# Kernel tuning notes

Hardware: AMD Instinct MI355X
Metric: run time of the kernel (lower is better)

## Reference

```python
import jax, jax.numpy as jnp
import numpy as np

S, B, E, H = 2048, 2, 1024, 16
D = E // H


def setup_inputs() -> dict:
    key = jax.random.key(0)
    k1, k2, k3, k4 = jax.random.split(key, 4)
    x = jax.random.normal(k1, (S, B, E), dtype=jnp.float32)
    # xavier_uniform for [3E, E] and [O, E]
    lim_qkv = float(np.sqrt(6.0 / (3 * E + E)))
    lim_out = float(np.sqrt(6.0 / (E + E)))
    w_qkv = jax.random.uniform(k2, (3 * E, E), jnp.float32, -lim_qkv, lim_qkv)
    b_qkv = jnp.zeros((3 * E,), jnp.float32)
    w_out = jax.random.uniform(k3, (E, E), jnp.float32, -lim_out, lim_out)
    b_out = jnp.zeros((E,), jnp.float32)
    return {"x": x, "w_qkv": w_qkv, "b_qkv": b_qkv, "w_out": w_out, "b_out": b_out}


def reference(x, w_qkv, b_qkv, w_out, b_out):
    # x: [S, B, E] (seq-first, as in the torch module)
    s, b, e = x.shape
    scaling = jnp.asarray(np.sqrt(D), x.dtype)
    qkv = jnp.einsum('sbe,fe->sbf', x, w_qkv) + b_qkv          # [S,B,3E]
    q, k, v = jnp.split(qkv, 3, axis=-1)
    q = q.reshape(s, b, H, D)
    k = k.reshape(s, b, H, D)
    v = v.reshape(s, b, H, D)
    # scores [B,H,S,S]; note original divides by sqrt(head_dim)
    scores = jnp.einsum('sbhd,tbhd->bhst', q, k) / scaling
    attn_w = jax.nn.softmax(scores.astype(jnp.float32), axis=-1).astype(scores.dtype)
    # dropout p=0.1 is identity in eval mode (training=False)
    attn = jnp.einsum('bhst,tbhd->sbhd', attn_w, v).reshape(s, b, e)
    out = jnp.einsum('sbe,oe->sbo', attn, w_out) + b_out        # [S,B,O]
    attn_avg = attn_w.mean(axis=1)                              # [B,S,S]
    return out, attn_avg
```

## Files before the change

kernel.cpp:

```cpp
#include <hip/hip_runtime.h>

#define SEQ   2048
#define BATCH 2
#define NH    16
#define HD    64
#define EMB   1024

#define QSCALE 0.18033688011112042f

using bf16x8 = __attribute__((ext_vector_type(8))) short;
using f32x4  = __attribute__((ext_vector_type(4))) float;
using f32x16 = __attribute__((ext_vector_type(16))) float;

__device__ __forceinline__ unsigned short f2bf(float f) {
  unsigned int u = __float_as_uint(f);
  u += 0x7FFFu + ((u >> 16) & 1u);
  return (unsigned short)(u >> 16);
}
__device__ __forceinline__ unsigned pk_bf16(float lo, float hi) {
  unsigned r;
  asm("v_cvt_pk_bf16_f32 %0, %1, %2" : "=v"(r) : "v"(lo), "v"(hi));
  return r;
}
__device__ __forceinline__ void gload16(const void* g, void* l) {
  __builtin_amdgcn_global_load_lds(
      (const __attribute__((address_space(1))) unsigned int*)g,
      (__attribute__((address_space(3))) unsigned int*)l, 16, 0, 0);
}

__global__ __launch_bounds__(256) void cvt_f32_bf16(const float* __restrict__ in,
                                                    unsigned short* __restrict__ out,
                                                    int n4) {
  int i = blockIdx.x * 256 + threadIdx.x;
  if (i < n4) {
    float4 v = reinterpret_cast<const float4*>(in)[i];
    ushort4 o;
    o.x = f2bf(v.x); o.y = f2bf(v.y); o.z = f2bf(v.z); o.w = f2bf(v.w);
    reinterpret_cast<ushort4*>(out)[i] = o;
  }
}

template <int EPI>
__global__ __launch_bounds__(256) void gemm_bt(
    const unsigned short* __restrict__ A,
    const unsigned short* __restrict__ B,
    const float* __restrict__ bias,
    float* __restrict__ Cf,
    unsigned short* __restrict__ Qb,
    unsigned short* __restrict__ Kb,
    unsigned short* __restrict__ VTb,
    int M, int N, int K) {
  __shared__ int4 As[128][8];
  __shared__ int4 Bs[128][8];
  const int tid = threadIdx.x;
  const int wid = tid >> 6, lane = tid & 63;
  const int wm = wid >> 1, wn = wid & 1;
  const int lg = lane >> 4, lr = lane & 15;
  const int lr8 = lane >> 3;
  const int lc8 = (lane & 7) ^ lr8;
  const int row0 = blockIdx.x * 128, col0 = blockIdx.y * 128;
  f32x4 acc[4][4] = {};
  for (int k0 = 0; k0 < K; k0 += 64) {
#pragma unroll
    for (int i = 0; i < 4; i++) {
      const int rb = wid * 32 + i * 8;
      gload16(&A[(size_t)(row0 + rb + lr8) * K + k0 + lc8 * 8], &As[rb][0]);
      gload16(&B[(size_t)(col0 + rb + lr8) * K + k0 + lc8 * 8], &Bs[rb][0]);
    }
    __syncthreads();
#pragma unroll
    for (int ks = 0; ks < 2; ks++) {
      bf16x8 af[4], bfr[4];
#pragma unroll
      for (int mi = 0; mi < 4; mi++) {
        int r = wm * 64 + mi * 16 + lr;
        af[mi] = *reinterpret_cast<const bf16x8*>(&As[r][(ks * 4 + lg) ^ (r & 7)]);
      }
#pragma unroll
      for (int ni = 0; ni < 4; ni++) {
        int r = wn * 64 + ni * 16 + lr;
        bfr[ni] = *reinterpret_cast<const bf16x8*>(&Bs[r][(ks * 4 + lg) ^ (r & 7)]);
      }
#pragma unroll
      for (int mi = 0; mi < 4; mi++)
#pragma unroll
        for (int ni = 0; ni < 4; ni++)
          acc[mi][ni] = __builtin_amdgcn_mfma_f32_16x16x32_bf16(af[mi], bfr[ni], acc[mi][ni], 0, 0, 0);
    }
    __syncthreads();
  }
#pragma unroll
  for (int mi = 0; mi < 4; mi++)
#pragma unroll
    for (int ni = 0; ni < 4; ni++) {
      const int row_b = row0 + wm * 64 + mi * 16 + lg * 4;
      const int col = col0 + wn * 64 + ni * 16 + lr;
      const float bs = bias[col];
      float v0 = acc[mi][ni][0] + bs;
      float v1 = acc[mi][ni][1] + bs;
      float v2 = acc[mi][ni][2] + bs;
      float v3 = acc[mi][ni][3] + bs;
      if (EPI == 0) {
        Cf[(size_t)(row_b + 0) * N + col] = v0;
        Cf[(size_t)(row_b + 1) * N + col] = v1;
        Cf[(size_t)(row_b + 2) * N + col] = v2;
        Cf[(size_t)(row_b + 3) * N + col] = v3;
      } else {
        const int which = col >> 10, rr = col & 1023;
        const int hh = rr >> 6, d = rr & 63;
        if (which == 2) {
          const int s0 = row_b >> 1;
          ushort2 p0; p0.x = f2bf(v0); p0.y = f2bf(v2);
          ushort2 p1; p1.x = f2bf(v1); p1.y = f2bf(v3);
          *reinterpret_cast<ushort2*>(&VTb[((size_t)((0 * NH + hh) * HD + d)) * SEQ + s0]) = p0;
          *reinterpret_cast<ushort2*>(&VTb[((size_t)((1 * NH + hh) * HD + d)) * SEQ + s0]) = p1;
        } else {
          unsigned short* dst = which == 0 ? Qb : Kb;
          const float sc = (which == 0) ? QSCALE : 1.0f;
          float vv[4] = {v0 * sc, v1 * sc, v2 * sc, v3 * sc};
#pragma unroll
          for (int r = 0; r < 4; r++) {
            int s = (row_b + r) >> 1, bb = r & 1;
            dst[(size_t)((bb * NH + hh) * SEQ + s) * HD + d] = f2bf(vv[r]);
          }
        }
      }
    }
}

__global__ __launch_bounds__(256, 2) void attn1(
    const unsigned short* __restrict__ Qb,
    const unsigned short* __restrict__ Kb,
    const unsigned short* __restrict__ VTb,
    unsigned short* __restrict__ attn_bf,
    float* __restrict__ lbuf) {
  __shared__ int4 Kt[2][64][8];
  __shared__ int4 Vt[2][64][8];
  const int tid = threadIdx.x;
  const int wid = tid >> 6, lane = tid & 63;
  const int l31 = lane & 31, lhi = lane >> 5;
  const int lr8 = lane >> 3;
  const int lc8 = (lane & 7) ^ lr8;
  const int L = blockIdx.x;
  const int v = (L & 7) * 64 + (L >> 3);
  const int bh = v >> 4, stile = v & 15;
  const int b = bh >> 4, h = bh & 15;
  const int s0 = stile * 128 + wid * 32;
  const unsigned short* Qg = Qb + (size_t)bh * SEQ * HD;
  const unsigned short* Kg = Kb + (size_t)bh * SEQ * HD;
  const unsigned short* VTg = VTb + (size_t)bh * HD * SEQ;

  bf16x8 qf[4];
#pragma unroll
  for (int ks = 0; ks < 4; ks++)
    qf[ks] = *reinterpret_cast<const bf16x8*>(Qg + (size_t)(s0 + l31) * HD + ks * 16 + lhi * 8);

  auto stage = [&](int tg, int buf) {
#pragma unroll
    for (int i = 0; i < 2; i++) {
      const int rb = wid * 16 + i * 8;
      gload16(Kg + (size_t)(tg * 64 + rb + lr8) * HD + lc8 * 8, &Kt[buf][rb][0]);
      gload16(VTg + (size_t)(rb + lr8) * SEQ + tg * 64 + lc8 * 8, &Vt[buf][rb][0]);
    }
  };

  const f32x16 fz = {};
  f32x16 o[2] = {};
  float ls = 0.f;
  bf16x8 paq[4];
  bf16x8 vfr[2][4];

  auto qk = [&](int cur, f32x16 st[2]) {
#pragma unroll
    for (int ti = 0; ti < 2; ti++) {
      const int row = ti * 32 + l31;
      bf16x8 kf = *reinterpret_cast<const bf16x8*>(&Kt[cur][row][(lhi) ^ (row & 7)]);
      st[ti] = __builtin_amdgcn_mfma_f32_32x32x16_bf16(kf, qf[0], fz, 0, 0, 0);
    }
#pragma unroll
    for (int ks = 1; ks < 4; ks++)
#pragma unroll
      for (int ti = 0; ti < 2; ti++) {
        const int row = ti * 32 + l31;
        bf16x8 kf = *reinterpret_cast<const bf16x8*>(&Kt[cur][row][(ks * 2 + lhi) ^ (row & 7)]);
        st[ti] = __builtin_amdgcn_mfma_f32_32x32x16_bf16(kf, qf[ks], st[ti], 0, 0, 0);
      }
  };
  auto softpack = [&](const f32x16 st[2]) {
    float p[32];
    float psum = 0.f;
#pragma unroll
    for (int ti = 0; ti < 2; ti++)
#pragma unroll
      for (int r = 0; r < 16; r++) {
        float e = __builtin_amdgcn_exp2f(st[ti][r]);
        p[ti * 16 + r] = e;
        psum += e;
      }
    ls += psum;
#pragma unroll
    for (int c = 0; c < 4; c++) {
      const int ti = c >> 1, cc = c & 1;
      const int pb = ti * 16 + cc * 8;
      unsigned w0 = pk_bf16(p[pb + 0], p[pb + 1]);
      unsigned w1 = pk_bf16(p[pb + 2], p[pb + 3]);
      unsigned w2 = pk_bf16(p[pb + 4], p[pb + 5]);
      unsigned w3 = pk_bf16(p[pb + 6], p[pb + 7]);
      asm volatile("v_permlane32_swap_b32 %0, %1" : "+v"(w0), "+v"(w2));
      asm volatile("v_permlane32_swap_b32 %0, %1" : "+v"(w1), "+v"(w3));
      union { unsigned u[4]; bf16x8 v; } pa;
      pa.u[0] = w0; pa.u[1] = w1; pa.u[2] = w2; pa.u[3] = w3;
      paq[c] = pa.v;
    }
  };
  auto loadv = [&](int cur) {
#pragma unroll
    for (int dt = 0; dt < 2; dt++)
#pragma unroll
      for (int c = 0; c < 4; c++) {
        const int row = dt * 32 + l31;
        vfr[dt][c] = *reinterpret_cast<const bf16x8*>(&Vt[cur][row][(c * 2 + lhi) ^ (row & 7)]);
      }
  };

  stage(0, 0);
  __syncthreads();

  {
    stage(1, 1);
    f32x16 st[2];
    __builtin_amdgcn_s_setprio(1);
    qk(0, st);
    __builtin_amdgcn_s_setprio(0);
    softpack(st);
    loadv(0);
    __syncthreads();
  }

  for (int t = 1; t < 32; t++) {
    const int cur = t & 1;
    if (t + 1 < 32) stage(t + 1, cur ^ 1);
    f32x16 st[2];
    __builtin_amdgcn_s_setprio(1);
#pragma unroll
    for (int c = 0; c < 4; c++)
#pragma unroll
      for (int dt = 0; dt < 2; dt++)
        o[dt] = __builtin_amdgcn_mfma_f32_32x32x16_bf16(paq[c], vfr[dt][c], o[dt], 0, 0, 0);
    qk(cur, st);
    __builtin_amdgcn_s_setprio(0);
    softpack(st);
    loadv(cur);
    __syncthreads();
  }
#pragma unroll
  for (int c = 0; c < 4; c++)
#pragma unroll
    for (int dt = 0; dt < 2; dt++)
      o[dt] = __builtin_amdgcn_mfma_f32_32x32x16_bf16(paq[c], vfr[dt][c], o[dt], 0, 0, 0);

  ls += __shfl_xor(ls, 32, 64);
  if (lhi == 0)
    lbuf[(size_t)bh * SEQ + s0 + l31] = ls;

#pragma unroll
  for (int r = 0; r < 16; r++) {
    const int s_off = (r & 3) + 8 * (r >> 2) + 4 * lhi;
    float denom = __shfl(ls, s_off, 64);
    float inv = __builtin_amdgcn_rcpf(denom);
    const int s = s0 + s_off;
#pragma unroll
    for (int dt = 0; dt < 2; dt++) {
      float ov = o[dt][r] * inv;
      attn_bf[((size_t)s * BATCH + b) * EMB + h * HD + dt * 32 + l31] = f2bf(ov);
    }
  }
}

__global__ __launch_bounds__(256) void attn2(
    const unsigned short* __restrict__ Qb,
    const unsigned short* __restrict__ Kb,
    const float* __restrict__ lbuf,
    float* __restrict__ avg_out) {
  const int b = blockIdx.z;
  const int s0 = blockIdx.y * 64;
  const int tc0 = blockIdx.x * 256;
  __shared__ int4 Qs[64][8];
  __shared__ int4 Ks[2][64][8];
  __shared__ float lls[NH][64];
  const int tid = threadIdx.x;
  const int wid = tid >> 6, lane = tid & 63;
  const int wm = wid >> 1, wn = wid & 1;
  const int lg = lane >> 4, lr = lane & 15;
  const int lr8 = lane >> 3;
  const int lc8 = (lane & 7) ^ lr8;

  for (int i = tid; i < NH * 64; i += 256) {
    int hh = i >> 6, r = i & 63;
    lls[hh][r] = 1.0f / ((float)NH * lbuf[(b * NH + hh) * SEQ + s0 + r]);
  }

  const size_t bh0 = (size_t)(b * NH) * SEQ;

  auto stageK = [&](const unsigned short* src, int buf) {
#pragma unroll
    for (int i = 0; i < 2; i++) {
      const int rb = wid * 16 + i * 8;
      gload16(src + (size_t)(rb + lr8) * HD + lc8 * 8, &Ks[buf][rb][0]);
    }
  };
  auto stageQ = [&](const unsigned short* src) {
#pragma unroll
    for (int i = 0; i < 2; i++) {
      const int rb = wid * 16 + i * 8;
      gload16(src + (size_t)(rb + lr8) * HD + lc8 * 8, &Qs[rb][0]);
    }
  };

  stageQ(Qb + (bh0 + s0) * HD);
  stageK(Kb + (bh0 + tc0) * HD, 0);
  __syncthreads();

  const f32x4 fz4 = {};
  f32x4 avg[4][2][2] = {};

  for (int h = 0; h < NH; h++) {
    bf16x8 af[2][2];
#pragma unroll
    for (int mi = 0; mi < 2; mi++) {
      int r = wm * 32 + mi * 16 + lr;
#pragma unroll
      for (int ks = 0; ks < 2; ks++)
        af[mi][ks] = *reinterpret_cast<const bf16x8*>(&Qs[r][(ks * 4 + lg) ^ (r & 7)]);
    }
    float linv[2][4];
#pragma unroll
    for (int mi = 0; mi < 2; mi++)
#pragma unroll
      for (int r = 0; r < 4; r++)
        linv[mi][r] = lls[h][wm * 32 + mi * 16 + lg * 4 + r];

    const unsigned short* Kgh = Kb + (bh0 + (size_t)h * SEQ + tc0) * HD;

    for (int t0 = 0; t0 < 4; t0++) {
      const int cur = t0 & 1;
      if (t0 < 3) {
        stageK(Kgh + (size_t)(t0 + 1) * 64 * HD, cur ^ 1);
      } else if (h + 1 < NH) {
        stageK(Kb + (bh0 + (size_t)(h + 1) * SEQ + tc0) * HD, cur ^ 1);
        stageQ(Qb + (bh0 + (size_t)(h + 1) * SEQ + s0) * HD);
      }
      f32x4 sacc[2][2];
      __builtin_amdgcn_s_setprio(1);
#pragma unroll
      for (int ks = 0; ks < 2; ks++) {
        bf16x8 bk[2];
#pragma unroll
        for (int ni = 0; ni < 2; ni++) {
          int rk = wn * 32 + ni * 16 + lr;
          bk[ni] = *reinterpret_cast<const bf16x8*>(&Ks[cur][rk][(ks * 4 + lg) ^ (rk & 7)]);
        }
#pragma unroll
        for (int mi = 0; mi < 2; mi++)
#pragma unroll
          for (int ni = 0; ni < 2; ni++)
            sacc[mi][ni] = __builtin_amdgcn_mfma_f32_16x16x32_bf16(
                af[mi][ks], bk[ni], ks == 0 ? fz4 : sacc[mi][ni], 0, 0, 0);
      }
      __builtin_amdgcn_s_setprio(0);
#pragma unroll
      for (int mi = 0; mi < 2; mi++)
#pragma unroll
        for (int ni = 0; ni < 2; ni++)
#pragma unroll
          for (int r = 0; r < 4; r++)
            avg[t0][mi][ni][r] += __builtin_amdgcn_exp2f(sacc[mi][ni][r]) * linv[mi][r];
      __syncthreads();
    }
  }

#pragma unroll
  for (int t0 = 0; t0 < 4; t0++)
#pragma unroll
    for (int mi = 0; mi < 2; mi++)
#pragma unroll
      for (int ni = 0; ni < 2; ni++)
#pragma unroll
        for (int r = 0; r < 4; r++) {
          int s = s0 + wm * 32 + mi * 16 + lg * 4 + r;
          int t = tc0 + t0 * 64 + wn * 32 + ni * 16 + lr;
          avg_out[((size_t)b * SEQ + s) * SEQ + t] = avg[t0][mi][ni][r];
        }
}

extern "C" void kernel_launch(void* const* d_in, const int* in_sizes, int n_in,
                              void* d_out, int out_size, void* d_ws, size_t ws_size,
                              hipStream_t stream) {
  const float* x     = (const float*)d_in[0];
  const float* w_qkv = (const float*)d_in[1];
  const float* b_qkv = (const float*)d_in[2];
  const float* w_out = (const float*)d_in[3];
  const float* b_out = (const float*)d_in[4];
  float* out = (float*)d_out;
  float* avg = out + (size_t)SEQ * BATCH * EMB;

  char* ws = (char*)d_ws;
  size_t off = 0;
  unsigned short* x_bf    = (unsigned short*)(ws + off); off += (size_t)SEQ * BATCH * EMB * 2;
  unsigned short* wqkv_bf = (unsigned short*)(ws + off); off += (size_t)3 * EMB * EMB * 2;
  unsigned short* wout_bf = (unsigned short*)(ws + off); off += (size_t)EMB * EMB * 2;
  unsigned short* Qbuf    = (unsigned short*)(ws + off); off += (size_t)BATCH * NH * SEQ * HD * 2;
  unsigned short* Kbuf    = (unsigned short*)(ws + off); off += (size_t)BATCH * NH * SEQ * HD * 2;
  unsigned short* VTbuf   = (unsigned short*)(ws + off); off += (size_t)BATCH * NH * HD * SEQ * 2;
  unsigned short* attn_bf = (unsigned short*)(ws + off); off += (size_t)SEQ * BATCH * EMB * 2;
  float*          lbuf    = (float*)(ws + off);          off += (size_t)BATCH * NH * SEQ * 4;

  cvt_f32_bf16<<<(SEQ * BATCH * EMB / 4) / 256, 256, 0, stream>>>(x, x_bf, SEQ * BATCH * EMB / 4);
  cvt_f32_bf16<<<(3 * EMB * EMB / 4) / 256, 256, 0, stream>>>(w_qkv, wqkv_bf, 3 * EMB * EMB / 4);
  cvt_f32_bf16<<<(EMB * EMB / 4) / 256, 256, 0, stream>>>(w_out, wout_bf, EMB * EMB / 4);

  gemm_bt<1><<<dim3(SEQ * BATCH / 128, 3 * EMB / 128), 256, 0, stream>>>(
      x_bf, wqkv_bf, b_qkv, nullptr, Qbuf, Kbuf, VTbuf, SEQ * BATCH, 3 * EMB, EMB);

  attn1<<<512, 256, 0, stream>>>(Qbuf, Kbuf, VTbuf, attn_bf, lbuf);

  attn2<<<dim3(SEQ / 256, SEQ / 64, BATCH), 256, 0, stream>>>(Qbuf, Kbuf, lbuf, avg);

  gemm_bt<0><<<dim3(SEQ * BATCH / 128, EMB / 128), 256, 0, stream>>>(
      attn_bf, wout_bf, b_out, out, nullptr, nullptr, nullptr, SEQ * BATCH, EMB, EMB);
}
```

Measured before the change: 152.9 us.

## Shrink attn2 tiles to 64x64, load Q fragments directly, fuse conversion kernels

The attention-average kernel now gives each block a 64-column key tile instead of 256 columns. That quadruples the grid and cuts the per-thread accumulators from 64 to 16 floats, with launch bounds asking for 4 blocks per CU. Q fragments are now read straight from global memory into registers and double-buffered across heads, so the shared-memory Q stage is gone. The three fp32-to-bf16 conversion launches are merged into one kernel to save launch overhead. In exchange, Q loads are replicated across more blocks and each block's QK work per barrier is smaller.

```diff
diff --git a/kernel.cpp b/kernel.cpp
--- a/kernel.cpp
+++ b/kernel.cpp
@@ -28,16 +28,24 @@
       (__attribute__((address_space(3))) unsigned int*)l, 16, 0, 0);
 }
 
-__global__ __launch_bounds__(256) void cvt_f32_bf16(const float* __restrict__ in,
-                                                    unsigned short* __restrict__ out,
-                                                    int n4) {
+__global__ __launch_bounds__(256) void cvt3_f32_bf16(
+    const float* __restrict__ a, int na4,
+    const float* __restrict__ b, int nb4,
+    const float* __restrict__ c, int nc4,
+    unsigned short* __restrict__ oa,
+    unsigned short* __restrict__ ob,
+    unsigned short* __restrict__ oc) {
   int i = blockIdx.x * 256 + threadIdx.x;
-  if (i < n4) {
-    float4 v = reinterpret_cast<const float4*>(in)[i];
-    ushort4 o;
-    o.x = f2bf(v.x); o.y = f2bf(v.y); o.z = f2bf(v.z); o.w = f2bf(v.w);
-    reinterpret_cast<ushort4*>(out)[i] = o;
-  }
+  const float* src;
+  unsigned short* dst;
+  int j = i;
+  if (j < na4) { src = a; dst = oa; }
+  else if ((j -= na4) < nb4) { src = b; dst = ob; }
+  else { j -= nb4; if (j >= nc4) return; src = c; dst = oc; }
+  float4 v = reinterpret_cast<const float4*>(src)[j];
+  ushort4 o;
+  o.x = f2bf(v.x); o.y = f2bf(v.y); o.z = f2bf(v.z); o.w = f2bf(v.w);
+  reinterpret_cast<ushort4*>(dst)[j] = o;
 }
 
 template <int EPI>
@@ -277,15 +285,14 @@
   }
 }
 
-__global__ __launch_bounds__(256) void attn2(
+__global__ __launch_bounds__(256, 4) void attn2(
     const unsigned short* __restrict__ Qb,
     const unsigned short* __restrict__ Kb,
     const float* __restrict__ lbuf,
     float* __restrict__ avg_out) {
   const int b = blockIdx.z;
   const int s0 = blockIdx.y * 64;
-  const int tc0 = blockIdx.x * 256;
-  __shared__ int4 Qs[64][8];
+  const int tc0 = blockIdx.x * 64;
   __shared__ int4 Ks[2][64][8];
   __shared__ float lls[NH][64];
   const int tid = threadIdx.x;
@@ -294,103 +301,95 @@
   const int lg = lane >> 4, lr = lane & 15;
   const int lr8 = lane >> 3;
   const int lc8 = (lane & 7) ^ lr8;
+  const size_t bh0 = (size_t)(b * NH) * SEQ;
 
   for (int i = tid; i < NH * 64; i += 256) {
     int hh = i >> 6, r = i & 63;
     lls[hh][r] = 1.0f / ((float)NH * lbuf[(b * NH + hh) * SEQ + s0 + r]);
   }
 
-  const size_t bh0 = (size_t)(b * NH) * SEQ;
-
-  auto stageK = [&](const unsigned short* src, int buf) {
+  auto stageK = [&](int h, int buf) {
+    const unsigned short* src = Kb + (bh0 + (size_t)h * SEQ + tc0) * HD;
 #pragma unroll
     for (int i = 0; i < 2; i++) {
       const int rb = wid * 16 + i * 8;
       gload16(src + (size_t)(rb + lr8) * HD + lc8 * 8, &Ks[buf][rb][0]);
     }
   };
-  auto stageQ = [&](const unsigned short* src) {
-#pragma unroll
-    for (int i = 0; i < 2; i++) {
-      const int rb = wid * 16 + i * 8;
-      gload16(src + (size_t)(rb + lr8) * HD + lc8 * 8, &Qs[rb][0]);
-    }
-  };
-
-  stageQ(Qb + (bh0 + s0) * HD);
-  stageK(Kb + (bh0 + tc0) * HD, 0);
+  auto loadQ = [&](int h, bf16x8 (&af)[2][2]) {
+    const unsigned short* Qgh = Qb + (bh0 + (size_t)h * SEQ) * HD;
+#pragma unroll
+    for (int mi = 0; mi < 2; mi++)
+#pragma unroll
+      for (int ks = 0; ks < 2; ks++)
+        af[mi][ks] = *reinterpret_cast<const bf16x8*>(
+            Qgh + (size_t)(s0 + wm * 32 + mi * 16 + lr) * HD + ks * 32 + lg * 8);
+  };
+
+  const f32x4 fz4 = {};
+  f32x4 avg[2][2] = {};
+  bf16x8 afA[2][2], afB[2][2];
+
+  stageK(0, 0);
+  loadQ(0, afA);
   __syncthreads();
 
-  const f32x4 fz4 = {};
-  f32x4 avg[4][2][2] = {};
-
-  for (int h = 0; h < NH; h++) {
-    bf16x8 af[2][2];
-#pragma unroll
-    for (int mi = 0; mi < 2; mi++) {
-      int r = wm * 32 + mi * 16 + lr;
-#pragma unroll
-      for (int ks = 0; ks < 2; ks++)
-        af[mi][ks] = *reinterpret_cast<const bf16x8*>(&Qs[r][(ks * 4 + lg) ^ (r & 7)]);
-    }
+  auto hiter = [&](int h, bf16x8 (&afc)[2][2], bf16x8 (&afn)[2][2]) {
+    const int cur = h & 1;
+    if (h + 1 < NH) {
+      stageK(h + 1, cur ^ 1);
+      loadQ(h + 1, afn);
+    }
+    f32x4 sacc[2][2];
+    __builtin_amdgcn_s_setprio(1);
+#pragma unroll
+    for (int ks = 0; ks < 2; ks++) {
+      bf16x8 bk[2];
+#pragma unroll
+      for (int ni = 0; ni < 2; ni++) {
+        int rk = wn * 32 + ni * 16 + lr;
+        bk[ni] = *reinterpret_cast<const bf16x8*>(&Ks[cur][rk][(ks * 4 + lg) ^ (rk & 7)]);
+      }
+#pragma unroll
+      for (int mi = 0; mi < 2; mi++)
+#pragma unroll
+        for (int ni = 0; ni < 2; ni++)
+          sacc[mi][ni] = __builtin_amdgcn_mfma_f32_16x16x32_bf16(
+              afc[mi][ks], bk[ni], ks == 0 ? fz4 : sacc[mi][ni], 0, 0, 0);
+    }
+    __builtin_amdgcn_s_setprio(0);
     float linv[2][4];
 #pragma unroll
     for (int mi = 0; mi < 2; mi++)
 #pragma unroll
       for (int r = 0; r < 4; r++)
         linv[mi][r] = lls[h][wm * 32 + mi * 16 + lg * 4 + r];
-
-    const unsigned short* Kgh = Kb + (bh0 + (size_t)h * SEQ + tc0) * HD;
-
-    for (int t0 = 0; t0 < 4; t0++) {
-      const int cur = t0 & 1;
-      if (t0 < 3) {
-        stageK(Kgh + (size_t)(t0 + 1) * 64 * HD, cur ^ 1);
-      } else if (h + 1 < NH) {
-        stageK(Kb + (bh0 + (size_t)(h + 1) * SEQ + tc0) * HD, cur ^ 1);
-        stageQ(Qb + (bh0 + (size_t)(h + 1) * SEQ + s0) * HD);
-      }
-      f32x4 sacc[2][2];
-      __builtin_amdgcn_s_setprio(1);
-#pragma unroll
-      for (int ks = 0; ks < 2; ks++) {
-        bf16x8 bk[2];
-#pragma unroll
-        for (int ni = 0; ni < 2; ni++) {
-          int rk = wn * 32 + ni * 16 + lr;
-          bk[ni] = *reinterpret_cast<const bf16x8*>(&Ks[cur][rk][(ks * 4 + lg) ^ (rk & 7)]);
-        }
-#pragma unroll
-        for (int mi = 0; mi < 2; mi++)
-#pragma unroll
-          for (int ni = 0; ni < 2; ni++)
-            sacc[mi][ni] = __builtin_amdgcn_mfma_f32_16x16x32_bf16(
-                af[mi][ks], bk[ni], ks == 0 ? fz4 : sacc[mi][ni], 0, 0, 0);
-      }
-      __builtin_amdgcn_s_setprio(0);
-#pragma unroll
-      for (int mi = 0; mi < 2; mi++)
-#pragma unroll
-        for (int ni = 0; ni < 2; ni++)
-#pragma unroll
-          for (int r = 0; r < 4; r++)
-            avg[t0][mi][ni][r] += __builtin_amdgcn_exp2f(sacc[mi][ni][r]) * linv[mi][r];
-      __syncthreads();
-    }
-  }
-
-#pragma unroll
-  for (int t0 = 0; t0 < 4; t0++)
 #pragma unroll
     for (int mi = 0; mi < 2; mi++)
 #pragma unroll
       for (int ni = 0; ni < 2; ni++)
 #pragma unroll
-        for (int r = 0; r < 4; r++) {
-          int s = s0 + wm * 32 + mi * 16 + lg * 4 + r;
-          int t = tc0 + t0 * 64 + wn * 32 + ni * 16 + lr;
-          avg_out[((size_t)b * SEQ + s) * SEQ + t] = avg[t0][mi][ni][r];
-        }
+        for (int r = 0; r < 4; r++)
+          avg[mi][ni][r] += __builtin_amdgcn_exp2f(sacc[mi][ni][r]) * linv[mi][r];
+    __syncthreads();
+  };
+
+#pragma unroll 1
+  for (int hp = 0; hp < NH / 2; hp++) {
+    hiter(2 * hp, afA, afB);
+    hiter(2 * hp + 1, afB, afA);
+  }
+
+#pragma unroll
+  for (int mi = 0; mi < 2; mi++)
+#pragma unroll
+    for (int ni = 0; ni < 2; ni++)
+#pragma unroll
+      for (int r = 0; r < 4; r++) {
+        int s = s0 + wm * 32 + mi * 16 + lg * 4 + r;
+        int t = tc0 + wn * 32 + ni * 16 + lr;
+        avg_out[((size_t)b * SEQ + s) * SEQ + t] = avg[mi][ni][r];
+      }
 }
 
 extern "C" void kernel_launch(void* const* d_in, const int* in_sizes, int n_in,
@@ -415,16 +414,21 @@
   unsigned short* attn_bf = (unsigned short*)(ws + off); off += (size_t)SEQ * BATCH * EMB * 2;
   float*          lbuf    = (float*)(ws + off);          off += (size_t)BATCH * NH * SEQ * 4;
 
-  cvt_f32_bf16<<<(SEQ * BATCH * EMB / 4) / 256, 256, 0, stream>>>(x, x_bf, SEQ * BATCH * EMB / 4);
-  cvt_f32_bf16<<<(3 * EMB * EMB / 4) / 256, 256, 0, stream>>>(w_qkv, wqkv_bf, 3 * EMB * EMB / 4);
-  cvt_f32_bf16<<<(EMB * EMB / 4) / 256, 256, 0, stream>>>(w_out, wout_bf, EMB * EMB / 4);
+  {
+    const int na4 = SEQ * BATCH * EMB / 4;
+    const int nb4 = 3 * EMB * EMB / 4;
+    const int nc4 = EMB * EMB / 4;
+    const int nblk = (na4 + nb4 + nc4 + 255) / 256;
+    cvt3_f32_bf16<<<nblk, 256, 0, stream>>>(x, na4, w_qkv, nb4, w_out, nc4,
+                                            x_bf, wqkv_bf, wout_bf);
+  }
 
   gemm_bt<1><<<dim3(SEQ * BATCH / 128, 3 * EMB / 128), 256, 0, stream>>>(
       x_bf, wqkv_bf, b_qkv, nullptr, Qbuf, Kbuf, VTbuf, SEQ * BATCH, 3 * EMB, EMB);
 
   attn1<<<512, 256, 0, stream>>>(Qbuf, Kbuf, VTbuf, attn_bf, lbuf);
 
-  attn2<<<dim3(SEQ / 256, SEQ / 64, BATCH), 256, 0, stream>>>(Qbuf, Kbuf, lbuf, avg);
+  attn2<<<dim3(SEQ / 64, SEQ / 64, BATCH), 256, 0, stream>>>(Qbuf, Kbuf, lbuf, avg);
 
   gemm_bt<0><<<dim3(SEQ * BATCH / 128, EMB / 128), 256, 0, stream>>>(
       attn_bf, wout_bf, b_out, out, nullptr, nullptr, nullptr, SEQ * BATCH, EMB, EMB);
```

New measurement: 183.6 us. 20.1% more time.
